# Optimization experiments

Measured on AMD Instinct MI355X. Metric: run time of the kernel, lower is better.

Reference implementation:

```python
import jax, jax.numpy as jnp
import numpy as np

N = 4096      # nodes
F = 512       # nfeat
D = 64        # nhid per head
H = 8         # nheads
C = 40        # nclass
ALPHA = 0.2   # leakyrelu slope
NEG = -1e9    # mask value (finite for bf16/fp16 safety; exp -> 0)
EDGE_P = 0.004


def setup_inputs() -> dict:
    key = jax.random.key(0)
    ks = jax.random.split(key, 8)
    x = jax.random.normal(ks[0], (N, F), jnp.float32)
    adj = jax.random.uniform(ks[1], (N, N)) < EDGE_P
    adj = adj | jnp.eye(N, dtype=bool)  # self-loops: every softmax row valid
    init = lambda k, shape, fan: jax.random.normal(k, shape, jnp.float32) / np.sqrt(fan)
    W1 = init(ks[2], (H, F, D), F)        # per-head tran.weight^T
    a1_src = init(ks[3], (H, D), D)       # att1 (j / source term)
    a1_dst = init(ks[4], (H, D), D)       # att2 (i / destination term)
    W2 = init(ks[5], (H * D, C), H * D)   # output head tran
    a2_src = init(ks[6], (C,), C)
    a2_dst = init(ks[7], (C,), C)
    return dict(x=x, adj=adj, W1=W1, a1_src=a1_src, a1_dst=a1_dst,
                W2=W2, a2_src=a2_src, a2_dst=a2_dst)


def reference(x, adj, W1, a1_src, a1_dst, W2, a2_src, a2_dst):
    # ---- layer 1: H heads in parallel (dropout = identity in eval) ----
    h = jnp.einsum('nf,hfd->hnd', x, W1)              # [H,N,D]
    si = jnp.einsum('hnd,hd->hn', h, a1_dst)          # att2(h): i term
    sj = jnp.einsum('hnd,hd->hn', h, a1_src)          # att1(h): j term
    e = jax.nn.leaky_relu(si[:, :, None] + sj[:, None, :], ALPHA)  # [H,N,N]
    e = jnp.where(adj[None], e, NEG)                  # mask non-edges
    p = jax.nn.softmax(e, axis=-1)                    # softmax over neighbors j
    out = jnp.einsum('hij,hjd->hid', p, h)            # [H,N,D]
    # torch.cat(heads, dim=1) -> [N, H*D] with heads contiguous
    x2 = jax.nn.elu(jnp.transpose(out, (1, 0, 2)).reshape(N, H * D))
    # ---- output attention head ----
    h2 = x2 @ W2                                      # [N,C]
    e2 = jax.nn.leaky_relu((h2 @ a2_dst)[:, None] + (h2 @ a2_src)[None, :], ALPHA)
    e2 = jnp.where(adj, e2, NEG)
    p2 = jax.nn.softmax(e2, axis=-1)
    return p2 @ h2                                    # [N,C]
```

## Files before the change

kernel.cpp:

```cpp
#include <hip/hip_runtime.h>

#define NN 4096
#define FF 512
#define DD 64
#define HH 8
#define CC 40
#define HD (HH * DD)
#define CP 64
#define MAXDEG 128
#define ALPHA 0.2f

#define BM 64
#define BN 64
#define BK 16
#define SK2 8
#define KH2 (FF / SK2)

typedef __attribute__((ext_vector_type(8))) short bf16x8;
typedef __attribute__((ext_vector_type(4))) float f32x4;

__device__ __forceinline__ float bf2f(unsigned short u) {
    union { unsigned int i; float f; } v;
    v.i = ((unsigned int)u) << 16;
    return v.f;
}

__device__ __forceinline__ unsigned short f2bf(float f) {
    union { float f; unsigned int u; } v;
    v.f = f;
    unsigned int r = v.u + 0x7fffu + ((v.u >> 16) & 1u);
    return (unsigned short)(r >> 16);
}

__device__ __forceinline__ float wave_sum(float v) {
    #pragma unroll
    for (int off = 32; off; off >>= 1) v += __shfl_xor(v, off, 64);
    return v;
}

__device__ __forceinline__ float wave_max(float v) {
    #pragma unroll
    for (int off = 32; off; off >>= 1) v = fmaxf(v, __shfl_xor(v, off, 64));
    return v;
}

__device__ __forceinline__ float read_f(const void* src, int i, int isBf16) {
    if (isBf16) return bf2f(((const unsigned short*)src)[i]);
    return ((const float*)src)[i];
}

__global__ __launch_bounds__(256) void sniff_both(const unsigned char* __restrict__ adj,
                                                  const unsigned int* __restrict__ xw,
                                                  unsigned int* __restrict__ flagA,
                                                  unsigned int* __restrict__ flagF) {
    __shared__ int bad_s;
    if (threadIdx.x == 0) bad_s = 0;
    __syncthreads();
    int b = blockIdx.x;
    if (b < 16) {
        int i = b * 256 + threadIdx.x;
        if (adj[(size_t)i * (NN + 1)] == 0) bad_s = 1;
        __syncthreads();
        if (threadIdx.x == 0) atomicMin(flagA, bad_s ? 0u : 1u);
    } else {
        int bb = b - 16;
        int bad = 0;
        #pragma unroll
        for (int q = 0; q < 4; q++) {
            unsigned int w = xw[(bb * 4 + q) * 256 + threadIdx.x];
            unsigned int e0 = (w >> 7) & 0xffu;
            unsigned int e1 = (w >> 23) & 0xffu;
            if (e0 >= 0x90u || e1 >= 0x90u) bad = 1;
        }
        if (bad) bad_s = 1;
        __syncthreads();
        if (threadIdx.x == 0) atomicMin(flagF, bad_s ? 0u : 1u);
    }
}

__global__ __launch_bounds__(256) void cvt_all(const void* __restrict__ x,
                                               const void* __restrict__ W1,
                                               const void* __restrict__ W2,
                                               const void* __restrict__ a1s,
                                               const void* __restrict__ a1d,
                                               const void* __restrict__ a2s,
                                               const void* __restrict__ a2d,
                                               unsigned short* __restrict__ xh,
                                               unsigned short* __restrict__ xl,
                                               unsigned short* __restrict__ W1bth,
                                               unsigned short* __restrict__ W1btl,
                                               float* __restrict__ W2p,
                                               float* __restrict__ a1sf,
                                               float* __restrict__ a1df,
                                               float* __restrict__ a2sf,
                                               float* __restrict__ a2df,
                                               float* __restrict__ si,
                                               float* __restrict__ sj,
                                               const unsigned int* __restrict__ flagF) {
    int i = blockIdx.x * 256 + threadIdx.x;
    int bf = (int)*flagF;
    const int nX = NN * FF;
    const int nW1 = HH * FF * DD;
    const int nW2p = HD * CP;
    const int nA1 = HD;
    const int nSS = HH * NN;
    if (i < nX) {
        float v = read_f(x, i, bf);
        unsigned short h16 = f2bf(v);
        xh[i] = h16;
        xl[i] = f2bf(v - bf2f(h16));
        return;
    }
    i -= nX;
    if (i < nW1) {
        int hd = i / (FF * DD);
        int rem = i % (FF * DD);
        int f = rem / DD, d = rem % DD;
        float v = read_f(W1, i, bf);
        unsigned short h16 = f2bf(v);
        int idx = (hd * DD + d) * FF + f;
        W1bth[idx] = h16;
        W1btl[idx] = f2bf(v - bf2f(h16));
        return;
    }
    i -= nW1;
    if (i < nW2p) {
        int k = i / CP, c = i % CP;
        W2p[i] = (c < CC) ? read_f(W2, k * CC + c, bf) : 0.f;
        return;
    }
    i -= nW2p;
    if (i < nA1) { a1sf[i] = read_f(a1s, i, bf); return; }
    i -= nA1;
    if (i < nA1) { a1df[i] = read_f(a1d, i, bf); return; }
    i -= nA1;
    if (i < CC) { a2sf[i] = read_f(a2s, i, bf); return; }
    i -= CC;
    if (i < CC) { a2df[i] = read_f(a2d, i, bf); return; }
    i -= CC;
    if (i < nSS) { si[i] = 0.f; return; }
    i -= nSS;
    if (i < nSS) { sj[i] = 0.f; return; }
}

__global__ __launch_bounds__(256) void build_nbr(const unsigned char* __restrict__ adj,
                                                 const unsigned int* __restrict__ flagA,
                                                 int* __restrict__ nbr,
                                                 int* __restrict__ deg) {
    int i = blockIdx.x;
    __shared__ int cnt;
    if (threadIdx.x == 0) cnt = 0;
    __syncthreads();
    if (*flagA) {
        uint4 v = ((const uint4*)(adj + (size_t)i * NN))[threadIdx.x];
        unsigned int u[4] = { v.x, v.y, v.z, v.w };
        int base = threadIdx.x * 16;
        #pragma unroll
        for (int q = 0; q < 4; q++) {
            #pragma unroll
            for (int b = 0; b < 4; b++) {
                if ((u[q] >> (8 * b)) & 0xffu) {
                    int p = atomicAdd(&cnt, 1);
                    if (p < MAXDEG) nbr[(size_t)i * MAXDEG + p] = base + q * 4 + b;
                }
            }
        }
    } else {
        const int4* row = (const int4*)((const int*)adj + (size_t)i * NN);
        #pragma unroll
        for (int q = 0; q < 4; q++) {
            int idx4 = q * 256 + threadIdx.x;
            int4 v = row[idx4];
            int base = idx4 * 4;
            if (v.x) { int p = atomicAdd(&cnt, 1); if (p < MAXDEG) nbr[(size_t)i * MAXDEG + p] = base; }
            if (v.y) { int p = atomicAdd(&cnt, 1); if (p < MAXDEG) nbr[(size_t)i * MAXDEG + p] = base + 1; }
            if (v.z) { int p = atomicAdd(&cnt, 1); if (p < MAXDEG) nbr[(size_t)i * MAXDEG + p] = base + 2; }
            if (v.w) { int p = atomicAdd(&cnt, 1); if (p < MAXDEG) nbr[(size_t)i * MAXDEG + p] = base + 3; }
        }
    }
    __syncthreads();
    if (threadIdx.x == 0) deg[i] = min(cnt, MAXDEG);
}

__global__ __launch_bounds__(256) void l1_gemm(const unsigned short* __restrict__ xh,
                                               const unsigned short* __restrict__ xl,
                                               const unsigned short* __restrict__ W1bth,
                                               const unsigned short* __restrict__ W1btl,
                                               const float* __restrict__ a1sf,
                                               const float* __restrict__ a1df,
                                               unsigned short* __restrict__ hb,
                                               float* __restrict__ si,
                                               float* __restrict__ sj) {
    __shared__ __align__(16) unsigned short Ah[64][40];
    __shared__ __align__(16) unsigned short Al[64][40];
    __shared__ __align__(16) unsigned short Bh[64][40];
    __shared__ __align__(16) unsigned short Bl[64][40];

    int bm = blockIdx.x, hd = blockIdx.y;
    int tid = threadIdx.x;
    int wave = tid >> 6, lane = tid & 63;
    int wm = wave >> 1, wn = wave & 1;
    int lr = lane & 15, lg = lane >> 4;

    int srow = tid >> 2;
    int sseg = (tid & 3) * 8;

    const unsigned short* xA = xh + (size_t)(bm * 64 + srow) * FF + sseg;
    const unsigned short* xB = xl + (size_t)(bm * 64 + srow) * FF + sseg;
    const unsigned short* wA = W1bth + (size_t)(hd * 64 + srow) * FF + sseg;
    const unsigned short* wB = W1btl + (size_t)(hd * 64 + srow) * FF + sseg;

    f32x4 acc[2][2];
    #pragma unroll
    for (int r = 0; r < 2; r++)
        #pragma unroll
        for (int c = 0; c < 2; c++) acc[r][c] = (f32x4){0.f, 0.f, 0.f, 0.f};

    uint4 ra_h = *(const uint4*)(xA);
    uint4 ra_l = *(const uint4*)(xB);
    uint4 rb_h = *(const uint4*)(wA);
    uint4 rb_l = *(const uint4*)(wB);

    for (int kk = 0; kk < FF; kk += 32) {
        __syncthreads();
        *(uint4*)&Ah[srow][sseg] = ra_h;
        *(uint4*)&Al[srow][sseg] = ra_l;
        *(uint4*)&Bh[srow][sseg] = rb_h;
        *(uint4*)&Bl[srow][sseg] = rb_l;
        __syncthreads();

        int kn = (kk + 32 < FF) ? kk + 32 : kk;
        ra_h = *(const uint4*)(xA + kn);
        ra_l = *(const uint4*)(xB + kn);
        rb_h = *(const uint4*)(wA + kn);
        rb_l = *(const uint4*)(wB + kn);

        bf16x8 a_h0 = *(const bf16x8*)&Ah[wm * 32 + lr][lg * 8];
        bf16x8 a_h1 = *(const bf16x8*)&Ah[wm * 32 + 16 + lr][lg * 8];
        bf16x8 a_l0 = *(const bf16x8*)&Al[wm * 32 + lr][lg * 8];
        bf16x8 a_l1 = *(const bf16x8*)&Al[wm * 32 + 16 + lr][lg * 8];
        bf16x8 b_h0 = *(const bf16x8*)&Bh[wn * 32 + lr][lg * 8];
        bf16x8 b_h1 = *(const bf16x8*)&Bh[wn * 32 + 16 + lr][lg * 8];
        bf16x8 b_l0 = *(const bf16x8*)&Bl[wn * 32 + lr][lg * 8];
        bf16x8 b_l1 = *(const bf16x8*)&Bl[wn * 32 + 16 + lr][lg * 8];

        acc[0][0] = __builtin_amdgcn_mfma_f32_16x16x32_bf16(a_h0, b_h0, acc[0][0], 0, 0, 0);
        acc[0][1] = __builtin_amdgcn_mfma_f32_16x16x32_bf16(a_h0, b_h1, acc[0][1], 0, 0, 0);
        acc[1][0] = __builtin_amdgcn_mfma_f32_16x16x32_bf16(a_h1, b_h0, acc[1][0], 0, 0, 0);
        acc[1][1] = __builtin_amdgcn_mfma_f32_16x16x32_bf16(a_h1, b_h1, acc[1][1], 0, 0, 0);
        acc[0][0] = __builtin_amdgcn_mfma_f32_16x16x32_bf16(a_h0, b_l0, acc[0][0], 0, 0, 0);
        acc[0][1] = __builtin_amdgcn_mfma_f32_16x16x32_bf16(a_h0, b_l1, acc[0][1], 0, 0, 0);
        acc[1][0] = __builtin_amdgcn_mfma_f32_16x16x32_bf16(a_h1, b_l0, acc[1][0], 0, 0, 0);
        acc[1][1] = __builtin_amdgcn_mfma_f32_16x16x32_bf16(a_h1, b_l1, acc[1][1], 0, 0, 0);
        acc[0][0] = __builtin_amdgcn_mfma_f32_16x16x32_bf16(a_l0, b_h0, acc[0][0], 0, 0, 0);
        acc[0][1] = __builtin_amdgcn_mfma_f32_16x16x32_bf16(a_l0, b_h1, acc[0][1], 0, 0, 0);
        acc[1][0] = __builtin_amdgcn_mfma_f32_16x16x32_bf16(a_l1, b_h0, acc[1][0], 0, 0, 0);
        acc[1][1] = __builtin_amdgcn_mfma_f32_16x16x32_bf16(a_l1, b_h1, acc[1][1], 0, 0, 0);
    }

    float adv[2], asv[2];
    #pragma unroll
    for (int fc = 0; fc < 2; fc++) {
        adv[fc] = a1df[hd * DD + wn * 32 + fc * 16 + lr];
        asv[fc] = a1sf[hd * DD + wn * 32 + fc * 16 + lr];
    }
    #pragma unroll
    for (int fr = 0; fr < 2; fr++) {
        #pragma unroll
        for (int q = 0; q < 4; q++) {
            int row = bm * 64 + wm * 32 + fr * 16 + lg * 4 + q;
            int colb = hd * 64 + wn * 32;
            hb[(size_t)row * HD + colb + lr] = f2bf(acc[fr][0][q]);
            hb[(size_t)row * HD + colb + 16 + lr] = f2bf(acc[fr][1][q]);
            float pd = acc[fr][0][q] * adv[0] + acc[fr][1][q] * adv[1];
            float ps = acc[fr][0][q] * asv[0] + acc[fr][1][q] * asv[1];
            #pragma unroll
            for (int off = 1; off < 16; off <<= 1) {
                pd += __shfl_xor(pd, off, 64);
                ps += __shfl_xor(ps, off, 64);
            }
            if (lr == 0) {
                atomicAdd(&si[hd * NN + row], pd);
                atomicAdd(&sj[hd * NN + row], ps);
            }
        }
    }
}

__global__ __launch_bounds__(512) void l1_attn(const int* __restrict__ nbr,
                                               const int* __restrict__ deg,
                                               const unsigned short* __restrict__ hb,
                                               const float* __restrict__ si,
                                               const float* __restrict__ sj,
                                               float* __restrict__ x2) {
    int i = blockIdx.x;
    int tid = threadIdx.x;
    int hd = tid >> 6, lane = tid & 63;
    int d = deg[i];
    __shared__ int js[MAXDEG];
    __shared__ float wls[HH][MAXDEG];
    for (int k = tid; k < d; k += 512) js[k] = nbr[(size_t)i * MAXDEG + k];
    __syncthreads();

    float sii = si[hd * NN + i];
    const float* sjh = sj + (size_t)hd * NN;
    float m = -1e30f;
    for (int k = lane; k < d; k += 64) {
        float sc = sii + sjh[js[k]];
        sc = sc > 0.f ? sc : ALPHA * sc;
        wls[hd][k] = sc;
        m = fmaxf(m, sc);
    }
    m = wave_max(m);
    float s = 0.f;
    for (int k = lane; k < d; k += 64) {
        float e = expf(wls[hd][k] - m);
        wls[hd][k] = e;
        s += e;
    }
    s = fmaxf(wave_sum(s), 1e-30f);

    float acc = 0.f;
    int k = 0;
    for (; k + 8 <= d; k += 8) {
        float v0 = bf2f(hb[(size_t)js[k] * HD + tid]);
        float v1 = bf2f(hb[(size_t)js[k + 1] * HD + tid]);
        float v2 = bf2f(hb[(size_t)js[k + 2] * HD + tid]);
        float v3 = bf2f(hb[(size_t)js[k + 3] * HD + tid]);
        float v4 = bf2f(hb[(size_t)js[k + 4] * HD + tid]);
        float v5 = bf2f(hb[(size_t)js[k + 5] * HD + tid]);
        float v6 = bf2f(hb[(size_t)js[k + 6] * HD + tid]);
        float v7 = bf2f(hb[(size_t)js[k + 7] * HD + tid]);
        acc = fmaf(wls[hd][k], v0, acc);
        acc = fmaf(wls[hd][k + 1], v1, acc);
        acc = fmaf(wls[hd][k + 2], v2, acc);
        acc = fmaf(wls[hd][k + 3], v3, acc);
        acc = fmaf(wls[hd][k + 4], v4, acc);
        acc = fmaf(wls[hd][k + 5], v5, acc);
        acc = fmaf(wls[hd][k + 6], v6, acc);
        acc = fmaf(wls[hd][k + 7], v7, acc);
    }
    for (; k + 4 <= d; k += 4) {
        float v0 = bf2f(hb[(size_t)js[k] * HD + tid]);
        float v1 = bf2f(hb[(size_t)js[k + 1] * HD + tid]);
        float v2 = bf2f(hb[(size_t)js[k + 2] * HD + tid]);
        float v3 = bf2f(hb[(size_t)js[k + 3] * HD + tid]);
        acc = fmaf(wls[hd][k], v0, acc);
        acc = fmaf(wls[hd][k + 1], v1, acc);
        acc = fmaf(wls[hd][k + 2], v2, acc);
        acc = fmaf(wls[hd][k + 3], v3, acc);
    }
    for (; k < d; k++)
        acc = fmaf(wls[hd][k], bf2f(hb[(size_t)js[k] * HD + tid]), acc);
    acc /= s;
    float r = acc > 0.f ? acc : expm1f(acc);
    x2[(size_t)i * HD + tid] = r;
}

template <int KHs, int Nb>
__device__ __forceinline__ void gemm_body(const float* __restrict__ Ap,
                                          const float* __restrict__ Bp,
                                          float* __restrict__ Co,
                                          int tid, int bm) {
    __shared__ float As[BK][BM + 4];
    __shared__ float Bs[BK][BN + 4];
    int tm = tid >> 4, tn = tid & 15;
    int m0 = tm * 4, n0 = tn * 4;
    int ar = tid >> 2, ak = (tid & 3) * 4;
    int bk = tid >> 4, bq = (tid & 15) * 4;

    float acc[4][4];
    #pragma unroll
    for (int r = 0; r < 4; r++)
        #pragma unroll
        for (int c = 0; c < 4; c++) acc[r][c] = 0.f;

    const float* Ar = Ap + (size_t)ar * FF;
    float4 av = *(const float4*)(Ar + ak);
    float4 bv = *(const float4*)(Bp + (size_t)bk * Nb + bq);

    for (int k0 = 0; k0 < KHs; k0 += BK) {
        __syncthreads();
        As[ak + 0][ar] = av.x;
        As[ak + 1][ar] = av.y;
        As[ak + 2][ar] = av.z;
        As[ak + 3][ar] = av.w;
        *(float4*)&Bs[bk][bq] = bv;
        __syncthreads();

        int kn = (k0 + BK < KHs) ? k0 + BK : k0;
        av = *(const float4*)(Ar + kn + ak);
        bv = *(const float4*)(Bp + (size_t)(kn + bk) * Nb + bq);

        #pragma unroll
        for (int k = 0; k < BK; k++) {
            float4 a = *(const float4*)&As[k][m0];
            float4 b = *(const float4*)&Bs[k][n0];
            acc[0][0] = fmaf(a.x, b.x, acc[0][0]);
            acc[0][1] = fmaf(a.x, b.y, acc[0][1]);
            acc[0][2] = fmaf(a.x, b.z, acc[0][2]);
            acc[0][3] = fmaf(a.x, b.w, acc[0][3]);
            acc[1][0] = fmaf(a.y, b.x, acc[1][0]);
            acc[1][1] = fmaf(a.y, b.y, acc[1][1]);
            acc[1][2] = fmaf(a.y, b.z, acc[1][2]);
            acc[1][3] = fmaf(a.y, b.w, acc[1][3]);
            acc[2][0] = fmaf(a.z, b.x, acc[2][0]);
            acc[2][1] = fmaf(a.z, b.y, acc[2][1]);
            acc[2][2] = fmaf(a.z, b.z, acc[2][2]);
            acc[2][3] = fmaf(a.z, b.w, acc[2][3]);
            acc[3][0] = fmaf(a.w, b.x, acc[3][0]);
            acc[3][1] = fmaf(a.w, b.y, acc[3][1]);
            acc[3][2] = fmaf(a.w, b.z, acc[3][2]);
            acc[3][3] = fmaf(a.w, b.w, acc[3][3]);
        }
    }

    #pragma unroll
    for (int r = 0; r < 4; r++) {
        float4 v = make_float4(acc[r][0], acc[r][1], acc[r][2], acc[r][3]);
        *(float4*)(Co + (size_t)(bm * BM + m0 + r) * Nb + n0) = v;
    }
}

__global__ __launch_bounds__(256) void l2_gemm(const float* __restrict__ x2,
                                               const float* __restrict__ W2p,
                                               float* __restrict__ Cp2) {
    int bm = blockIdx.x, sk = blockIdx.z;
    gemm_body<KH2, CP>(x2 + (size_t)bm * BM * FF + sk * KH2,
                       W2p + (size_t)(sk * KH2) * CP,
                       Cp2 + (size_t)sk * NN * CP,
                       threadIdx.x, bm);
}

__global__ __launch_bounds__(64) void l2_post(const float* __restrict__ Cp2,
                                              const float* __restrict__ a2sf,
                                              const float* __restrict__ a2df,
                                              float* __restrict__ h2,
                                              float* __restrict__ d1,
                                              float* __restrict__ d2) {
    int n = blockIdx.x, c = threadIdx.x;
    float v = 0.f;
    #pragma unroll
    for (int sk = 0; sk < SK2; sk++)
        v += Cp2[(size_t)sk * NN * CP + (size_t)n * CP + c];
    if (c < CC) h2[(size_t)n * CC + c] = v;
    float pd = wave_sum((c < CC) ? v * a2df[c] : 0.f);
    float ps = wave_sum((c < CC) ? v * a2sf[c] : 0.f);
    if (c == 0) {
        d1[n] = pd;
        d2[n] = ps;
    }
}

__global__ __launch_bounds__(256) void l2_attn(const int* __restrict__ nbr,
                                               const int* __restrict__ deg,
                                               const float* __restrict__ h2,
                                               const float* __restrict__ d1,
                                               const float* __restrict__ d2,
                                               float* __restrict__ out) {
    int w = threadIdx.x >> 6, lane = threadIdx.x & 63;
    int i = blockIdx.x * 4 + w;
    int d = deg[i];
    __shared__ int js[4][MAXDEG];
    __shared__ float wls[4][MAXDEG];
    for (int k = lane; k < d; k += 64) js[w][k] = nbr[(size_t)i * MAXDEG + k];

    float sii = d1[i];
    float m = -1e30f;
    for (int k = lane; k < d; k += 64) {
        float sc = sii + d2[js[w][k]];
        sc = sc > 0.f ? sc : ALPHA * sc;
        wls[w][k] = sc;
        m = fmaxf(m, sc);
    }
    m = wave_max(m);
    float s = 0.f;
    for (int k = lane; k < d; k += 64) {
        float e = expf(wls[w][k] - m);
        wls[w][k] = e;
        s += e;
    }
    s = fmaxf(wave_sum(s), 1e-30f);

    int c = lane;
    if (c < CC) {
        float acc = 0.f;
        int k = 0;
        for (; k + 4 <= d; k += 4) {
            float v0 = h2[(size_t)js[w][k] * CC + c];
            float v1 = h2[(size_t)js[w][k + 1] * CC + c];
            float v2 = h2[(size_t)js[w][k + 2] * CC + c];
            float v3 = h2[(size_t)js[w][k + 3] * CC + c];
            acc = fmaf(wls[w][k], v0, acc);
            acc = fmaf(wls[w][k + 1], v1, acc);
            acc = fmaf(wls[w][k + 2], v2, acc);
            acc = fmaf(wls[w][k + 3], v3, acc);
        }
        for (; k < d; k++)
            acc = fmaf(wls[w][k], h2[(size_t)js[w][k] * CC + c], acc);
        out[(size_t)i * CC + c] = acc / s;
    }
}

extern "C" void kernel_launch(void* const* d_in, const int* in_sizes, int n_in,
                              void* d_out, int out_size, void* d_ws, size_t ws_size,
                              hipStream_t stream) {
    const void* x   = d_in[0];
    const unsigned char* adj = (const unsigned char*)d_in[1];
    const void* W1  = d_in[2];
    const void* a1s = d_in[3];
    const void* a1d = d_in[4];
    const void* W2  = d_in[5];
    const void* a2s = d_in[6];
    const void* a2d = d_in[7];

    char* ws = (char*)d_ws;
    int*   nbr   = (int*)(ws + 0);
    int*   deg   = (int*)(ws + 2097152);
    float* si    = (float*)(ws + 2113536);
    float* sj    = (float*)(ws + 2244608);
    unsigned short* xh    = (unsigned short*)(ws + 2375680);
    unsigned short* xl    = (unsigned short*)(ws + 6569984);
    unsigned short* W1bth = (unsigned short*)(ws + 10764288);
    unsigned short* W1btl = (unsigned short*)(ws + 11288576);
    float* W2p   = (float*)(ws + 11812864);
    float* a1sf  = (float*)(ws + 11943936);
    float* a1df  = (float*)(ws + 11945984);
    float* a2sf  = (float*)(ws + 11948032);
    float* a2df  = (float*)(ws + 11948288);
    unsigned int* flagA = (unsigned int*)(ws + 11948544);
    unsigned int* flagF = (unsigned int*)(ws + 11948548);
    unsigned short* hb = (unsigned short*)(ws + 11948800);
    float* x2    = (float*)(ws + 16143104);
    float* h2    = (float*)(ws + 24531712);
    float* d1    = (float*)(ws + 25187072);
    float* d2    = (float*)(ws + 25203456);
    float* Cp2   = (float*)(ws + 25219840);

    hipLaunchKernelGGL(sniff_both, dim3(80), dim3(256), 0, stream,
                       adj, (const unsigned int*)x, flagA, flagF);

    const int nCvt = NN * FF + HH * FF * DD + HD * CP + 2 * HD + 2 * CC
                   + 2 * HH * NN;
    hipLaunchKernelGGL(cvt_all, dim3((nCvt + 255) / 256), dim3(256), 0, stream,
                       x, W1, W2, a1s, a1d, a2s, a2d,
                       xh, xl, W1bth, W1btl, W2p, a1sf, a1df, a2sf, a2df,
                       si, sj, flagF);

    hipLaunchKernelGGL(build_nbr, dim3(NN), dim3(256), 0, stream, adj, flagA, nbr, deg);
    hipLaunchKernelGGL(l1_gemm, dim3(NN / 64, HH), dim3(256), 0, stream,
                       xh, xl, W1bth, W1btl, a1sf, a1df, hb, si, sj);
    hipLaunchKernelGGL(l1_attn, dim3(NN), dim3(512), 0, stream,
                       nbr, deg, hb, si, sj, x2);
    hipLaunchKernelGGL(l2_gemm, dim3(NN / BM, 1, SK2), dim3(256), 0, stream,
                       x2, W2p, Cp2);
    hipLaunchKernelGGL(l2_post, dim3(NN), dim3(64), 0, stream,
                       Cp2, a2sf, a2df, h2, d1, d2);
    hipLaunchKernelGGL(l2_attn, dim3(NN / 4), dim3(256), 0, stream,
                       nbr, deg, h2, d1, d2, (float*)d_out);
}
```

Measured before the change: 171.2 us.

## Fuse x bf16 split into GEMM, inline dtype sniffing, pack attention loads

```diff
diff --git a/kernel.cpp b/kernel.cpp
--- a/kernel.cpp
+++ b/kernel.cpp
@@ -49,33 +49,21 @@
     return ((const float*)src)[i];
 }
 
-__global__ __launch_bounds__(256) void sniff_both(const unsigned char* __restrict__ adj,
-                                                  const unsigned int* __restrict__ xw,
-                                                  unsigned int* __restrict__ flagA,
-                                                  unsigned int* __restrict__ flagF) {
-    __shared__ int bad_s;
-    if (threadIdx.x == 0) bad_s = 0;
-    __syncthreads();
-    int b = blockIdx.x;
-    if (b < 16) {
-        int i = b * 256 + threadIdx.x;
-        if (adj[(size_t)i * (NN + 1)] == 0) bad_s = 1;
-        __syncthreads();
-        if (threadIdx.x == 0) atomicMin(flagA, bad_s ? 0u : 1u);
-    } else {
-        int bb = b - 16;
-        int bad = 0;
-        #pragma unroll
-        for (int q = 0; q < 4; q++) {
-            unsigned int w = xw[(bb * 4 + q) * 256 + threadIdx.x];
-            unsigned int e0 = (w >> 7) & 0xffu;
-            unsigned int e1 = (w >> 23) & 0xffu;
-            if (e0 >= 0x90u || e1 >= 0x90u) bad = 1;
-        }
-        if (bad) bad_s = 1;
-        __syncthreads();
-        if (threadIdx.x == 0) atomicMin(flagF, bad_s ? 0u : 1u);
-    }
+__device__ __forceinline__ int sniff_x(const void* xraw, int tid, int* fS) {
+    if (tid == 0) *fS = 1;
+    __syncthreads();
+    int bad = 0;
+    const unsigned int* xw = (const unsigned int*)xraw;
+    #pragma unroll
+    for (int q = 0; q < 4; q++) {
+        unsigned int w = xw[(tid & 255) * 4 + q];
+        unsigned int e0 = (w >> 7) & 0xffu;
+        unsigned int e1 = (w >> 23) & 0xffu;
+        if (e0 >= 0x90u || e1 >= 0x90u) bad = 1;
+    }
+    if (bad) *fS = 0;
+    __syncthreads();
+    return *fS;
 }
 
 __global__ __launch_bounds__(256) void cvt_all(const void* __restrict__ x,
@@ -85,8 +73,6 @@
                                                const void* __restrict__ a1d,
                                                const void* __restrict__ a2s,
                                                const void* __restrict__ a2d,
-                                               unsigned short* __restrict__ xh,
-                                               unsigned short* __restrict__ xl,
                                                unsigned short* __restrict__ W1bth,
                                                unsigned short* __restrict__ W1btl,
                                                float* __restrict__ W2p,
@@ -95,23 +81,14 @@
                                                float* __restrict__ a2sf,
                                                float* __restrict__ a2df,
                                                float* __restrict__ si,
-                                               float* __restrict__ sj,
-                                               const unsigned int* __restrict__ flagF) {
+                                               float* __restrict__ sj) {
+    __shared__ int fS;
+    int bf = sniff_x(x, threadIdx.x, &fS);
     int i = blockIdx.x * 256 + threadIdx.x;
-    int bf = (int)*flagF;
-    const int nX = NN * FF;
     const int nW1 = HH * FF * DD;
     const int nW2p = HD * CP;
     const int nA1 = HD;
     const int nSS = HH * NN;
-    if (i < nX) {
-        float v = read_f(x, i, bf);
-        unsigned short h16 = f2bf(v);
-        xh[i] = h16;
-        xl[i] = f2bf(v - bf2f(h16));
-        return;
-    }
-    i -= nX;
     if (i < nW1) {
         int hd = i / (FF * DD);
         int rem = i % (FF * DD);
@@ -144,14 +121,17 @@
 }
 
 __global__ __launch_bounds__(256) void build_nbr(const unsigned char* __restrict__ adj,
-                                                 const unsigned int* __restrict__ flagA,
                                                  int* __restrict__ nbr,
                                                  int* __restrict__ deg) {
+    __shared__ int cnt;
+    __shared__ int fS;
+    if (threadIdx.x == 0) { cnt = 0; fS = 1; }
+    __syncthreads();
+    if (adj[(size_t)threadIdx.x * (NN + 1)] == 0) fS = 0;
+    __syncthreads();
+    int isByte = fS;
     int i = blockIdx.x;
-    __shared__ int cnt;
-    if (threadIdx.x == 0) cnt = 0;
-    __syncthreads();
-    if (*flagA) {
+    if (isByte) {
         uint4 v = ((const uint4*)(adj + (size_t)i * NN))[threadIdx.x];
         unsigned int u[4] = { v.x, v.y, v.z, v.w };
         int base = threadIdx.x * 16;
@@ -182,8 +162,7 @@
     if (threadIdx.x == 0) deg[i] = min(cnt, MAXDEG);
 }
 
-__global__ __launch_bounds__(256) void l1_gemm(const unsigned short* __restrict__ xh,
-                                               const unsigned short* __restrict__ xl,
+__global__ __launch_bounds__(256) void l1_gemm(const void* __restrict__ xraw,
                                                const unsigned short* __restrict__ W1bth,
                                                const unsigned short* __restrict__ W1btl,
                                                const float* __restrict__ a1sf,
@@ -195,20 +174,20 @@
     __shared__ __align__(16) unsigned short Al[64][40];
     __shared__ __align__(16) unsigned short Bh[64][40];
     __shared__ __align__(16) unsigned short Bl[64][40];
+    __shared__ int fS;
 
     int bm = blockIdx.x, hd = blockIdx.y;
     int tid = threadIdx.x;
+    int isBf16 = sniff_x(xraw, tid, &fS);
+
     int wave = tid >> 6, lane = tid & 63;
     int wm = wave >> 1, wn = wave & 1;
     int lr = lane & 15, lg = lane >> 4;
-
     int srow = tid >> 2;
     int sseg = (tid & 3) * 8;
 
-    const unsigned short* xA = xh + (size_t)(bm * 64 + srow) * FF + sseg;
-    const unsigned short* xB = xl + (size_t)(bm * 64 + srow) * FF + sseg;
-    const unsigned short* wA = W1bth + (size_t)(hd * 64 + srow) * FF + sseg;
-    const unsigned short* wB = W1btl + (size_t)(hd * 64 + srow) * FF + sseg;
+    const unsigned short* wAp = W1bth + (size_t)(hd * 64 + srow) * FF + sseg;
+    const unsigned short* wBp = W1btl + (size_t)(hd * 64 + srow) * FF + sseg;
 
     f32x4 acc[2][2];
     #pragma unroll
@@ -216,46 +195,77 @@
         #pragma unroll
         for (int c = 0; c < 2; c++) acc[r][c] = (f32x4){0.f, 0.f, 0.f, 0.f};
 
-    uint4 ra_h = *(const uint4*)(xA);
-    uint4 ra_l = *(const uint4*)(xB);
-    uint4 rb_h = *(const uint4*)(wA);
-    uint4 rb_l = *(const uint4*)(wB);
-
-    for (int kk = 0; kk < FF; kk += 32) {
-        __syncthreads();
-        *(uint4*)&Ah[srow][sseg] = ra_h;
-        *(uint4*)&Al[srow][sseg] = ra_l;
-        *(uint4*)&Bh[srow][sseg] = rb_h;
-        *(uint4*)&Bl[srow][sseg] = rb_l;
-        __syncthreads();
-
-        int kn = (kk + 32 < FF) ? kk + 32 : kk;
-        ra_h = *(const uint4*)(xA + kn);
-        ra_l = *(const uint4*)(xB + kn);
-        rb_h = *(const uint4*)(wA + kn);
-        rb_l = *(const uint4*)(wB + kn);
-
-        bf16x8 a_h0 = *(const bf16x8*)&Ah[wm * 32 + lr][lg * 8];
-        bf16x8 a_h1 = *(const bf16x8*)&Ah[wm * 32 + 16 + lr][lg * 8];
-        bf16x8 a_l0 = *(const bf16x8*)&Al[wm * 32 + lr][lg * 8];
-        bf16x8 a_l1 = *(const bf16x8*)&Al[wm * 32 + 16 + lr][lg * 8];
-        bf16x8 b_h0 = *(const bf16x8*)&Bh[wn * 32 + lr][lg * 8];
-        bf16x8 b_h1 = *(const bf16x8*)&Bh[wn * 32 + 16 + lr][lg * 8];
-        bf16x8 b_l0 = *(const bf16x8*)&Bl[wn * 32 + lr][lg * 8];
-        bf16x8 b_l1 = *(const bf16x8*)&Bl[wn * 32 + 16 + lr][lg * 8];
-
-        acc[0][0] = __builtin_amdgcn_mfma_f32_16x16x32_bf16(a_h0, b_h0, acc[0][0], 0, 0, 0);
-        acc[0][1] = __builtin_amdgcn_mfma_f32_16x16x32_bf16(a_h0, b_h1, acc[0][1], 0, 0, 0);
-        acc[1][0] = __builtin_amdgcn_mfma_f32_16x16x32_bf16(a_h1, b_h0, acc[1][0], 0, 0, 0);
-        acc[1][1] = __builtin_amdgcn_mfma_f32_16x16x32_bf16(a_h1, b_h1, acc[1][1], 0, 0, 0);
-        acc[0][0] = __builtin_amdgcn_mfma_f32_16x16x32_bf16(a_h0, b_l0, acc[0][0], 0, 0, 0);
-        acc[0][1] = __builtin_amdgcn_mfma_f32_16x16x32_bf16(a_h0, b_l1, acc[0][1], 0, 0, 0);
-        acc[1][0] = __builtin_amdgcn_mfma_f32_16x16x32_bf16(a_h1, b_l0, acc[1][0], 0, 0, 0);
-        acc[1][1] = __builtin_amdgcn_mfma_f32_16x16x32_bf16(a_h1, b_l1, acc[1][1], 0, 0, 0);
-        acc[0][0] = __builtin_amdgcn_mfma_f32_16x16x32_bf16(a_l0, b_h0, acc[0][0], 0, 0, 0);
-        acc[0][1] = __builtin_amdgcn_mfma_f32_16x16x32_bf16(a_l0, b_h1, acc[0][1], 0, 0, 0);
-        acc[1][0] = __builtin_amdgcn_mfma_f32_16x16x32_bf16(a_l1, b_h0, acc[1][0], 0, 0, 0);
-        acc[1][1] = __builtin_amdgcn_mfma_f32_16x16x32_bf16(a_l1, b_h1, acc[1][1], 0, 0, 0);
+    if (isBf16) {
+        const unsigned short* xp = (const unsigned short*)xraw
+                                 + (size_t)(bm * 64 + srow) * FF + sseg;
+        uint4 ra = *(const uint4*)xp;
+        uint4 rb = *(const uint4*)wAp;
+        for (int kk = 0; kk < FF; kk += 32) {
+            __syncthreads();
+            *(uint4*)&Ah[srow][sseg] = ra;
+            *(uint4*)&Bh[srow][sseg] = rb;
+            __syncthreads();
+            int kn = (kk + 32 < FF) ? kk + 32 : kk;
+            ra = *(const uint4*)(xp + kn);
+            rb = *(const uint4*)(wAp + kn);
+            bf16x8 a0 = *(const bf16x8*)&Ah[wm * 32 + lr][lg * 8];
+            bf16x8 a1 = *(const bf16x8*)&Ah[wm * 32 + 16 + lr][lg * 8];
+            bf16x8 b0 = *(const bf16x8*)&Bh[wn * 32 + lr][lg * 8];
+            bf16x8 b1 = *(const bf16x8*)&Bh[wn * 32 + 16 + lr][lg * 8];
+            acc[0][0] = __builtin_amdgcn_mfma_f32_16x16x32_bf16(a0, b0, acc[0][0], 0, 0, 0);
+            acc[0][1] = __builtin_amdgcn_mfma_f32_16x16x32_bf16(a0, b1, acc[0][1], 0, 0, 0);
+            acc[1][0] = __builtin_amdgcn_mfma_f32_16x16x32_bf16(a1, b0, acc[1][0], 0, 0, 0);
+            acc[1][1] = __builtin_amdgcn_mfma_f32_16x16x32_bf16(a1, b1, acc[1][1], 0, 0, 0);
+        }
+    } else {
+        const float* xp = (const float*)xraw + (size_t)(bm * 64 + srow) * FF + sseg;
+        float4 ra0 = *(const float4*)xp;
+        float4 ra1 = *(const float4*)(xp + 4);
+        uint4 rbh = *(const uint4*)wAp;
+        uint4 rbl = *(const uint4*)wBp;
+        for (int kk = 0; kk < FF; kk += 32) {
+            __syncthreads();
+            union { unsigned short s[8]; uint4 v; } uh, ul;
+            float fv[8] = { ra0.x, ra0.y, ra0.z, ra0.w, ra1.x, ra1.y, ra1.z, ra1.w };
+            #pragma unroll
+            for (int q = 0; q < 8; q++) {
+                unsigned short h16 = f2bf(fv[q]);
+                uh.s[q] = h16;
+                ul.s[q] = f2bf(fv[q] - bf2f(h16));
+            }
+            *(uint4*)&Ah[srow][sseg] = uh.v;
+            *(uint4*)&Al[srow][sseg] = ul.v;
+            *(uint4*)&Bh[srow][sseg] = rbh;
+            *(uint4*)&Bl[srow][sseg] = rbl;
+            __syncthreads();
+            int kn = (kk + 32 < FF) ? kk + 32 : kk;
+            ra0 = *(const float4*)(xp + kn);
+            ra1 = *(const float4*)(xp + kn + 4);
+            rbh = *(const uint4*)(wAp + kn);
+            rbl = *(const uint4*)(wBp + kn);
+
+            bf16x8 a_h0 = *(const bf16x8*)&Ah[wm * 32 + lr][lg * 8];
+            bf16x8 a_h1 = *(const bf16x8*)&Ah[wm * 32 + 16 + lr][lg * 8];
+            bf16x8 a_l0 = *(const bf16x8*)&Al[wm * 32 + lr][lg * 8];
+            bf16x8 a_l1 = *(const bf16x8*)&Al[wm * 32 + 16 + lr][lg * 8];
+            bf16x8 b_h0 = *(const bf16x8*)&Bh[wn * 32 + lr][lg * 8];
+            bf16x8 b_h1 = *(const bf16x8*)&Bh[wn * 32 + 16 + lr][lg * 8];
+            bf16x8 b_l0 = *(const bf16x8*)&Bl[wn * 32 + lr][lg * 8];
+            bf16x8 b_l1 = *(const bf16x8*)&Bl[wn * 32 + 16 + lr][lg * 8];
+
+            acc[0][0] = __builtin_amdgcn_mfma_f32_16x16x32_bf16(a_h0, b_h0, acc[0][0], 0, 0, 0);
+            acc[0][1] = __builtin_amdgcn_mfma_f32_16x16x32_bf16(a_h0, b_h1, acc[0][1], 0, 0, 0);
+            acc[1][0] = __builtin_amdgcn_mfma_f32_16x16x32_bf16(a_h1, b_h0, acc[1][0], 0, 0, 0);
+            acc[1][1] = __builtin_amdgcn_mfma_f32_16x16x32_bf16(a_h1, b_h1, acc[1][1], 0, 0, 0);
+            acc[0][0] = __builtin_amdgcn_mfma_f32_16x16x32_bf16(a_h0, b_l0, acc[0][0], 0, 0, 0);
+            acc[0][1] = __builtin_amdgcn_mfma_f32_16x16x32_bf16(a_h0, b_l1, acc[0][1], 0, 0, 0);
+            acc[1][0] = __builtin_amdgcn_mfma_f32_16x16x32_bf16(a_h1, b_l0, acc[1][0], 0, 0, 0);
+            acc[1][1] = __builtin_amdgcn_mfma_f32_16x16x32_bf16(a_h1, b_l1, acc[1][1], 0, 0, 0);
+            acc[0][0] = __builtin_amdgcn_mfma_f32_16x16x32_bf16(a_l0, b_h0, acc[0][0], 0, 0, 0);
+            acc[0][1] = __builtin_amdgcn_mfma_f32_16x16x32_bf16(a_l0, b_h1, acc[0][1], 0, 0, 0);
+            acc[1][0] = __builtin_amdgcn_mfma_f32_16x16x32_bf16(a_l1, b_h0, acc[1][0], 0, 0, 0);
+            acc[1][1] = __builtin_amdgcn_mfma_f32_16x16x32_bf16(a_l1, b_h1, acc[1][1], 0, 0, 0);
+        }
     }
 
     float adv[2], asv[2];
@@ -287,7 +297,7 @@
     }
 }
 
-__global__ __launch_bounds__(512) void l1_attn(const int* __restrict__ nbr,
+__global__ __launch_bounds__(256) void l1_attn(const int* __restrict__ nbr,
                                                const int* __restrict__ deg,
                                                const unsigned short* __restrict__ hb,
                                                const float* __restrict__ si,
@@ -295,66 +305,66 @@
                                                float* __restrict__ x2) {
     int i = blockIdx.x;
     int tid = threadIdx.x;
-    int hd = tid >> 6, lane = tid & 63;
+    int wave = tid >> 6, lane = tid & 63;
     int d = deg[i];
     __shared__ int js[MAXDEG];
     __shared__ float wls[HH][MAXDEG];
-    for (int k = tid; k < d; k += 512) js[k] = nbr[(size_t)i * MAXDEG + k];
-    __syncthreads();
-
+    for (int k = tid; k < d; k += 256) js[k] = nbr[(size_t)i * MAXDEG + k];
+    __syncthreads();
+
+    int hd = wave * 2 + (lane >> 5);
+    int l32 = lane & 31;
     float sii = si[hd * NN + i];
     const float* sjh = sj + (size_t)hd * NN;
     float m = -1e30f;
-    for (int k = lane; k < d; k += 64) {
+    for (int k = l32; k < d; k += 32) {
         float sc = sii + sjh[js[k]];
         sc = sc > 0.f ? sc : ALPHA * sc;
         wls[hd][k] = sc;
         m = fmaxf(m, sc);
     }
-    m = wave_max(m);
+    #pragma unroll
+    for (int off = 16; off; off >>= 1) m = fmaxf(m, __shfl_xor(m, off, 64));
     float s = 0.f;
-    for (int k = lane; k < d; k += 64) {
+    for (int k = l32; k < d; k += 32) {
         float e = expf(wls[hd][k] - m);
         wls[hd][k] = e;
         s += e;
     }
-    s = fmaxf(wave_sum(s), 1e-30f);
-
-    float acc = 0.f;
+    #pragma unroll
+    for (int off = 16; off; off >>= 1) s += __shfl_xor(s, off, 64);
+    float inv = 1.f / fmaxf(s, 1e-30f);
+    for (int k = l32; k < d; k += 32) wls[hd][k] *= inv;
+    __syncthreads();
+
+    const unsigned int* hu = (const unsigned int*)hb;
+    const float* wl = wls[tid >> 5];
+    float a0 = 0.f, a1 = 0.f;
     int k = 0;
-    for (; k + 8 <= d; k += 8) {
-        float v0 = bf2f(hb[(size_t)js[k] * HD + tid]);
-        float v1 = bf2f(hb[(size_t)js[k + 1] * HD + tid]);
-        float v2 = bf2f(hb[(size_t)js[k + 2] * HD + tid]);
-        float v3 = bf2f(hb[(size_t)js[k + 3] * HD + tid]);
-        float v4 = bf2f(hb[(size_t)js[k + 4] * HD + tid]);
-        float v5 = bf2f(hb[(size_t)js[k + 5] * HD + tid]);
-        float v6 = bf2f(hb[(size_t)js[k + 6] * HD + tid]);
-        float v7 = bf2f(hb[(size_t)js[k + 7] * HD + tid]);
-        acc = fmaf(wls[hd][k], v0, acc);
-        acc = fmaf(wls[hd][k + 1], v1, acc);
-        acc = fmaf(wls[hd][k + 2], v2, acc);
-        acc = fmaf(wls[hd][k + 3], v3, acc);
-        acc = fmaf(wls[hd][k + 4], v4, acc);
-        acc = fmaf(wls[hd][k + 5], v5, acc);
-        acc = fmaf(wls[hd][k + 6], v6, acc);
-        acc = fmaf(wls[hd][k + 7], v7, acc);
-    }
     for (; k + 4 <= d; k += 4) {
-        float v0 = bf2f(hb[(size_t)js[k] * HD + tid]);
-        float v1 = bf2f(hb[(size_t)js[k + 1] * HD + tid]);
-        float v2 = bf2f(hb[(size_t)js[k + 2] * HD + tid]);
-        float v3 = bf2f(hb[(size_t)js[k + 3] * HD + tid]);
-        acc = fmaf(wls[hd][k], v0, acc);
-        acc = fmaf(wls[hd][k + 1], v1, acc);
-        acc = fmaf(wls[hd][k + 2], v2, acc);
-        acc = fmaf(wls[hd][k + 3], v3, acc);
-    }
-    for (; k < d; k++)
-        acc = fmaf(wls[hd][k], bf2f(hb[(size_t)js[k] * HD + tid]), acc);
-    acc /= s;
-    float r = acc > 0.f ? acc : expm1f(acc);
-    x2[(size_t)i * HD + tid] = r;
+        unsigned int v0 = hu[(size_t)js[k] * 256 + tid];
+        unsigned int v1 = hu[(size_t)js[k + 1] * 256 + tid];
+        unsigned int v2 = hu[(size_t)js[k + 2] * 256 + tid];
+        unsigned int v3 = hu[(size_t)js[k + 3] * 256 + tid];
+        float w0 = wl[k], w1 = wl[k + 1], w2 = wl[k + 2], w3 = wl[k + 3];
+        a0 = fmaf(w0, bf2f((unsigned short)v0), a0);
+        a1 = fmaf(w0, bf2f((unsigned short)(v0 >> 16)), a1);
+        a0 = fmaf(w1, bf2f((unsigned short)v1), a0);
+        a1 = fmaf(w1, bf2f((unsigned short)(v1 >> 16)), a1);
+        a0 = fmaf(w2, bf2f((unsigned short)v2), a0);
+        a1 = fmaf(w2, bf2f((unsigned short)(v2 >> 16)), a1);
+        a0 = fmaf(w3, bf2f((unsigned short)v3), a0);
+        a1 = fmaf(w3, bf2f((unsigned short)(v3 >> 16)), a1);
+    }
+    for (; k < d; k++) {
+        unsigned int v = hu[(size_t)js[k] * 256 + tid];
+        float w = wl[k];
+        a0 = fmaf(w, bf2f((unsigned short)v), a0);
+        a1 = fmaf(w, bf2f((unsigned short)(v >> 16)), a1);
+    }
+    float r0 = a0 > 0.f ? a0 : expm1f(a0);
+    float r1 = a1 > 0.f ? a1 : expm1f(a1);
+    *(float2*)(x2 + (size_t)i * HD + tid * 2) = make_float2(r0, r1);
 }
 
 template <int KHs, int Nb>
@@ -519,38 +529,29 @@
     int*   deg   = (int*)(ws + 2097152);
     float* si    = (float*)(ws + 2113536);
     float* sj    = (float*)(ws + 2244608);
-    unsigned short* xh    = (unsigned short*)(ws + 2375680);
-    unsigned short* xl    = (unsigned short*)(ws + 6569984);
-    unsigned short* W1bth = (unsigned short*)(ws + 10764288);
-    unsigned short* W1btl = (unsigned short*)(ws + 11288576);
-    float* W2p   = (float*)(ws + 11812864);
-    float* a1sf  = (float*)(ws + 11943936);
-    float* a1df  = (float*)(ws + 11945984);
-    float* a2sf  = (float*)(ws + 11948032);
-    float* a2df  = (float*)(ws + 11948288);
-    unsigned int* flagA = (unsigned int*)(ws + 11948544);
-    unsigned int* flagF = (unsigned int*)(ws + 11948548);
-    unsigned short* hb = (unsigned short*)(ws + 11948800);
-    float* x2    = (float*)(ws + 16143104);
-    float* h2    = (float*)(ws + 24531712);
-    float* d1    = (float*)(ws + 25187072);
-    float* d2    = (float*)(ws + 25203456);
-    float* Cp2   = (float*)(ws + 25219840);
-
-    hipLaunchKernelGGL(sniff_both, dim3(80), dim3(256), 0, stream,
-                       adj, (const unsigned int*)x, flagA, flagF);
-
-    const int nCvt = NN * FF + HH * FF * DD + HD * CP + 2 * HD + 2 * CC
-                   + 2 * HH * NN;
+    unsigned short* W1bth = (unsigned short*)(ws + 2375680);
+    unsigned short* W1btl = (unsigned short*)(ws + 2899968);
+    float* W2p   = (float*)(ws + 3424256);
+    float* a1sf  = (float*)(ws + 3555328);
+    float* a1df  = (float*)(ws + 3557376);
+    float* a2sf  = (float*)(ws + 3559424);
+    float* a2df  = (float*)(ws + 3559680);
+    unsigned short* hb = (unsigned short*)(ws + 3559936);
+    float* x2    = (float*)(ws + 7754240);
+    float* h2    = (float*)(ws + 16142848);
+    float* d1    = (float*)(ws + 16798208);
+    float* d2    = (float*)(ws + 16814592);
+    float* Cp2   = (float*)(ws + 16830976);
+
+    const int nCvt = HH * FF * DD + HD * CP + 2 * HD + 2 * CC + 2 * HH * NN;
     hipLaunchKernelGGL(cvt_all, dim3((nCvt + 255) / 256), dim3(256), 0, stream,
                        x, W1, W2, a1s, a1d, a2s, a2d,
-                       xh, xl, W1bth, W1btl, W2p, a1sf, a1df, a2sf, a2df,
-                       si, sj, flagF);
-
-    hipLaunchKernelGGL(build_nbr, dim3(NN), dim3(256), 0, stream, adj, flagA, nbr, deg);
+                       W1bth, W1btl, W2p, a1sf, a1df, a2sf, a2df, si, sj);
+
+    hipLaunchKernelGGL(build_nbr, dim3(NN), dim3(256), 0, stream, adj, nbr, deg);
     hipLaunchKernelGGL(l1_gemm, dim3(NN / 64, HH), dim3(256), 0, stream,
-                       xh, xl, W1bth, W1btl, a1sf, a1df, hb, si, sj);
-    hipLaunchKernelGGL(l1_attn, dim3(NN), dim3(512), 0, stream,
+                       x, W1bth, W1btl, a1sf, a1df, hb, si, sj);
+    hipLaunchKernelGGL(l1_attn, dim3(NN), dim3(256), 0, stream,
                        nbr, deg, hb, si, sj, x2);
     hipLaunchKernelGGL(l2_gemm, dim3(NN / BM, 1, SK2), dim3(256), 0, stream,
                        x2, W2p, Cp2);
```

New measurement: 166.5 us. -2.7%, faster.
